# Performance work log

Hardware: AMD Instinct MI355X
Metric: run time of the kernel (lower is better)

Reference implementation:

```python
import jax, jax.numpy as jnp
import numpy as np

BS, Q, S1, S2 = 8, 128, 32, 64
H_DIM, NH = 768, 12
DH = H_DIM // NH


def _linear_params(k, scale=0.02):
    kw, _ = jax.random.split(k)
    w = jax.random.normal(kw, (H_DIM, H_DIM), jnp.float32) * scale
    b = jnp.zeros((H_DIM,), jnp.float32)
    return w, b


def setup_inputs() -> dict:
    root = jax.random.key(0)
    ks = jax.random.split(root, 12)
    wq_w, wq_b = _linear_params(ks[0])
    wk_w, wk_b = _linear_params(ks[1])
    wv_w, wv_b = _linear_params(ks[2])
    sq_w, sq_b = _linear_params(ks[3])
    sk_w, sk_b = _linear_params(ks[4])
    sv_w, sv_b = _linear_params(ks[5])
    return {
        "q_in": jax.random.normal(ks[6], (BS, Q, H_DIM), jnp.float32),
        "k_in": jax.random.normal(ks[7], (BS, S1, S2, H_DIM), jnp.float32),
        "v_in": jax.random.normal(ks[8], (BS, S1, S2, H_DIM), jnp.float32),
        "kvec": jax.random.normal(ks[9], (BS, S1, H_DIM), jnp.float32),
        "word_mask": jnp.ones((BS, S1, S2), jnp.int32),
        "sentence_mask": jnp.ones((BS * Q, S1), jnp.int32),
        "wq_w": wq_w, "wq_b": wq_b, "wk_w": wk_w, "wk_b": wk_b,
        "wv_w": wv_w, "wv_b": wv_b, "sq_w": sq_w, "sq_b": sq_b,
        "sk_w": sk_w, "sk_b": sk_b, "sv_w": sv_w, "sv_b": sv_b,
    }


def reference(q_in, k_in, v_in, kvec, word_mask, sentence_mask,
              wq_w, wq_b, wk_w, wk_b, wv_w, wv_b,
              sq_w, sq_b, sk_w, sk_b, sv_w, sv_b):
    bs, q_len = q_in.shape[0], q_in.shape[1]
    s1, s2 = k_in.shape[1], k_in.shape[2]
    scale = 1.0 / jnp.sqrt(jnp.float32(DH))

    # additive masks, as in the torch module
    wm = (1.0 - word_mask.astype(jnp.float32)) * -10000.0      # [bs, s1, s2]
    sm = (1.0 - sentence_mask.astype(jnp.float32)) * -10000.0  # [bs*Q, s1]

    # ---- word-level attention ----
    q = (q_in @ wq_w + wq_b).reshape(bs, q_len, NH, DH)
    k = (k_in @ wk_w + wk_b).reshape(bs, s1, s2, NH, DH)
    v = (v_in @ wv_w + wv_b).reshape(bs, s1, s2, NH, DH)
    # scores over tokens within each sentence: [bs, s1, H, Q, s2]
    scores1 = jnp.einsum('bqhd,bsthd->bshqt', q, k) * scale
    probs1 = jax.nn.softmax(scores1 + wm[:, :, None, None, :], axis=-1)
    # word_hidden: [bs, Q, s1, h]
    wh = jnp.einsum('bshqt,bsthd->bqshd', probs1, v).reshape(bs, q_len, s1, H_DIM)

    # ---- sentence-level attention ----
    sq = (q_in @ sq_w + sq_b).reshape(bs, q_len, NH, DH)
    sk = (kvec @ sk_w + sk_b).reshape(bs, s1, NH, DH)   # shared across queries
    sv = (wh @ sv_w + sv_b).reshape(bs, q_len, s1, NH, DH)
    scores2 = jnp.einsum('bqhd,bshd->bqhs', sq, sk) * scale  # [bs, Q, H, s1]
    scores2 = scores2 + sm.reshape(bs, q_len, s1)[:, :, None, :]
    probs2 = jax.nn.softmax(scores2, axis=-1)
    out = jnp.einsum('bqhs,bqshd->bqhd', probs2, sv).reshape(bs * q_len, H_DIM)
    return out
```

## Files before the change

### kernel.cpp

```cpp
#include <hip/hip_runtime.h>
#include <hip/hip_bf16.h>


typedef __attribute__((ext_vector_type(8))) short short8;
typedef __attribute__((ext_vector_type(4))) short short4v;
typedef __attribute__((ext_vector_type(4))) float f32x4;

__device__ __forceinline__ short f2bf(float f) {
  __hip_bfloat16 b = __float2bfloat16(f);
  return __builtin_bit_cast(short, b);
}
__device__ __forceinline__ float bf2f(short s) {
  __hip_bfloat16 b = __builtin_bit_cast(__hip_bfloat16, s);
  return __bfloat162float(b);
}

#define MFMA16(a, b, c) __builtin_amdgcn_mfma_f32_16x16x32_bf16((a), (b), (c), 0, 0, 0)

__device__ __forceinline__ void async_load16(const void* g, void* l) {
  auto l3 = (__attribute__((address_space(3))) void*)(uintptr_t)(
      reinterpret_cast<uintptr_t>(l));
  auto g1 = (const __attribute__((address_space(1))) void*)g;
  __builtin_amdgcn_global_load_lds(g1, l3, 16, 0, 0);
}

#define KBAR()                                      \
  do {                                              \
    asm volatile("" ::: "memory");                  \
    __builtin_amdgcn_s_barrier();                   \
    asm volatile("" ::: "memory");                  \
  } while (0)
#define VMW(N) asm volatile("s_waitcnt vmcnt(" #N ")" ::: "memory")

__global__ __launch_bounds__(256)
void prep(const float* __restrict__ w0, const float* __restrict__ w1,
          const float* __restrict__ w2, const float* __restrict__ w3,
          const float* __restrict__ w4, const float* __restrict__ w5,
          short* __restrict__ WT,
          const float* __restrict__ q_in, const float* __restrict__ k_in,
          const float* __restrict__ v_in, const float* __restrict__ kvec,
          short* __restrict__ qbf, short* __restrict__ kbf,
          short* __restrict__ vbf, short* __restrict__ kvb) {
  const int id = blockIdx.x;
  const int tid = threadIdx.x;
  if (id < 3456) {
    __shared__ float tile[32][33];
    const int zz = id / 576, r = id % 576;
    const float* W = (zz == 0) ? w0 : (zz == 1) ? w1 : (zz == 2) ? w2
                   : (zz == 3) ? w3 : (zz == 4) ? w4 : w5;
    short* WTo = WT + (size_t)zz * 768 * 768;
    const int bx = (r % 24) * 32, by = (r / 24) * 32;
    const int tx = tid & 31, ty = tid >> 5;
    #pragma unroll
    for (int i = 0; i < 32; i += 8)
      tile[ty + i][tx] = W[(size_t)(by + ty + i) * 768 + bx + tx];
    __syncthreads();
    #pragma unroll
    for (int i = 0; i < 32; i += 8)
      WTo[(size_t)(bx + ty + i) * 768 + by + tx] = f2bf(tile[tx][ty + i]);
    return;
  }
  const int i = (id - 3456) * 256 + tid;
  const float* src;
  short* dst;
  int idx;
  if (i < 98304)        { src = q_in; dst = qbf; idx = i; }
  else if (i < 1671168) { src = k_in; dst = kbf; idx = i - 98304; }
  else if (i < 3244032) { src = v_in; dst = vbf; idx = i - 1671168; }
  else                  { src = kvec; dst = kvb; idx = i - 3244032; }
  const float4* s = (const float4*)src + (size_t)idx * 2;
  const float4 a = s[0], b = s[1];
  __align__(16) short tmp[8] = {f2bf(a.x), f2bf(a.y), f2bf(a.z), f2bf(a.w),
                                f2bf(b.x), f2bf(b.y), f2bf(b.z), f2bf(b.w)};
  *((short8*)dst + idx) = *(short8*)tmp;
}

__global__ __launch_bounds__(512, 2)
void gemm_proj(const short* __restrict__ kbf, const short* __restrict__ vbf,
               const short* __restrict__ qbf, const short* __restrict__ kvb,
               const short* __restrict__ WT6,
               const float* __restrict__ wk_b, const float* __restrict__ wv_b,
               const float* __restrict__ wq_b, const float* __restrict__ sq_b,
               const float* __restrict__ sk_b,
               short* __restrict__ kp, short* __restrict__ vT,
               short* __restrict__ qp, float* __restrict__ sqp,
               float* __restrict__ skp) {
  const int K = 768, WELEM = 768 * 768;
  extern __shared__ __align__(16) char smem_c[];
  short* smem = (short*)smem_c;
  const int tid = threadIdx.x;
  const int w = tid >> 6, lane = tid & 63, quad = lane >> 4, l16 = lane & 15;
  const f32x4 zero4 = {0.f, 0.f, 0.f, 0.f};

  if (blockIdx.z < 2) {
    short* LA = smem;
    short* LB = smem + 2 * 256 * 64;
    const int z = blockIdx.z;
    const short* Ag = z ? vbf : kbf;
    const short* Bg = z ? (WT6 + 3 * WELEM) : (WT6 + 2 * WELEM);
    const float* bias = z ? wv_b : wk_b;
    const int m0 = blockIdx.x * 256, n0 = blockIdx.y * 256;
    const int wr = w >> 2, wc = w & 3;

    const int srow = lane >> 3;
    const int schk = (lane & 7) ^ srow;
    const short* ag0 = Ag + (size_t)(m0 + w * 8 + srow) * K + schk * 8;
    const short* bg0 = Bg + (size_t)(n0 + w * 8 + srow) * K + schk * 8;
    short* la0 = LA + (w * 8) * 64;
    short* lb0 = LB + (w * 8) * 64;
    const int fsw = l16 & 7;

    f32x4 acc[8][4];
    #pragma unroll
    for (int i = 0; i < 8; i++)
      #pragma unroll
      for (int j = 0; j < 4; j++) acc[i][j] = zero4;

    auto STG1 = [&](int op, int h, int kt) {
      if (kt >= 12) kt -= 2;
      const int buf = kt & 1;
      const short* g = (op ? bg0 : ag0) + (size_t)h * 128 * K + (size_t)kt * 64;
      short* lb = (op ? lb0 : la0) + buf * 16384 + h * (128 * 64);
      async_load16(g, lb);
      async_load16(g + (size_t)64 * K, lb + 64 * 64);
    };

    short8 af[4][2];
    short8 bfr[2][2][2];

#define LDA_(BUF, IH)                                                        \
  _Pragma("unroll") for (int i = 0; i < 4; i++)                              \
    _Pragma("unroll") for (int kb = 0; kb < 2; kb++)                         \
      af[i][kb] = *(const short8*)&LA[(BUF)*16384 +                          \
          (wr * 128 + (IH)*64 + i * 16 + l16) * 64 +                         \
          (((kb * 4 + quad) ^ fsw) * 8)];
#define LDB_(BUF, JH)                                                        \
  _Pragma("unroll") for (int j = 0; j < 2; j++)                              \
    _Pragma("unroll") for (int kb = 0; kb < 2; kb++)                         \
      bfr[JH][j][kb] = *(const short8*)&LB[(BUF)*16384 +                     \
          (wc * 64 + (JH)*32 + j * 16 + l16) * 64 +                          \
          (((kb * 4 + quad) ^ fsw) * 8)];
#define MM_(IH, JH)                                                          \
  __builtin_amdgcn_s_setprio(1);                                             \
  _Pragma("unroll") for (int i = 0; i < 4; i++)                              \
    _Pragma("unroll") for (int j = 0; j < 2; j++) {                          \
      acc[(IH)*4 + i][(JH)*2 + j] =                                          \
          MFMA16(af[i][0], bfr[JH][j][0], acc[(IH)*4 + i][(JH)*2 + j]);      \
      acc[(IH)*4 + i][(JH)*2 + j] =                                          \
          MFMA16(af[i][1], bfr[JH][j][1], acc[(IH)*4 + i][(JH)*2 + j]);      \
    }                                                                        \
  __builtin_amdgcn_s_setprio(0);

    STG1(0, 0, 0); STG1(0, 1, 0); STG1(1, 0, 0); STG1(1, 1, 0);
    STG1(1, 0, 1); STG1(1, 1, 1);
    VMW(4);
    KBAR();

    #pragma unroll 1
    for (int it = 0; it < 6; ++it) {
      const int o = 2 * it + 1, e2 = 2 * it + 2, o2 = 2 * it + 3;
      LDA_(0, 0); LDB_(0, 0); STG1(0, 0, o); KBAR(); MM_(0, 0); KBAR();
      LDB_(0, 1); STG1(0, 1, o); KBAR(); MM_(0, 1); KBAR();
      LDA_(0, 1); STG1(1, 0, e2); KBAR(); MM_(1, 1); KBAR();
      STG1(1, 1, e2); KBAR(); MM_(1, 0); VMW(4); KBAR();
      LDA_(1, 0); LDB_(1, 0); STG1(0, 0, e2); KBAR(); MM_(0, 0); KBAR();
      LDB_(1, 1); STG1(0, 1, e2); KBAR(); MM_(0, 1); KBAR();
      LDA_(1, 1); STG1(1, 0, o2); KBAR(); MM_(1, 1); KBAR();
      STG1(1, 1, o2); KBAR(); MM_(1, 0); VMW(4); KBAR();
    }
#undef LDA_
#undef LDB_
#undef MM_
    VMW(0);

    if (z == 0) {
      #pragma unroll
      for (int I = 0; I < 8; I++)
        #pragma unroll
        for (int J = 0; J < 4; J++) {
          const int col = n0 + wc * 64 + J * 16 + l16;
          const float bv = bias[col];
          #pragma unroll
          for (int r = 0; r < 4; r++) {
            const int g = m0 + wr * 128 + I * 16 + quad * 4 + r;
            kp[(size_t)g * 768 + col] = f2bf(acc[I][J][r] + bv);
          }
        }
    } else {
      const int hh = (n0 >> 6) + wc;
      #pragma unroll
      for (int I = 0; I < 8; I++) {
        const int bs_ = (m0 >> 6) + wr * 2 + (I >> 2);
        const int t0 = (I & 3) * 16 + quad * 4;
        #pragma unroll
        for (int J = 0; J < 4; J++) {
          const int dd = J * 16 + l16;
          const float bv = bias[hh * 64 + dd];
          __align__(8) short tmp[4];
          #pragma unroll
          for (int r = 0; r < 4; r++) tmp[r] = f2bf(acc[I][J][r] + bv);
          *(short4v*)&vT[(((size_t)bs_ * 12 + hh) * 64 + dd) * 64 + t0] =
              *(short4v*)tmp;
        }
      }
    }
    return;
  }

  {
    const int id = blockIdx.x + 64 * blockIdx.y;
    if (id >= 108) return;
    short* As = smem;
    short* Bs = smem + 128 * 32;
    const int qmode = (id < 96);
    const int r = qmode ? id : (id - 96);
    const int bx = qmode ? (r % 8) : (r % 2);
    const int by = qmode ? (r / 8) : (r / 2);
    const short* A = qmode ? qbf : kvb;
    const short* WT = qmode ? (WT6 + 0 * WELEM) : (WT6 + 4 * WELEM);

    const int wm = (w >> 1) * 64, wn = (w & 1) * 64;
    const int m0 = bx * 128, n0 = by * 128;
    const int grow = w * 32 + (lane >> 2);
    const int kc = (lane & 3) * 8;
    const short* ag = A + (size_t)(m0 + grow) * K + kc;
    const short* bg = WT + (size_t)(n0 + grow) * K + kc;
    short* al = &As[(w * 32) * 32];
    short* bl = &Bs[(w * 32) * 32];

    f32x4 acc[4][4];
    #pragma unroll
    for (int i = 0; i < 4; i++)
      #pragma unroll
      for (int j = 0; j < 4; j++) acc[i][j] = zero4;

    for (int k0 = 0; k0 < K; k0 += 32) {
      __syncthreads();
      if (tid < 256) {
        async_load16(ag, al);
        async_load16(ag + (size_t)16 * K, al + 16 * 32);
        async_load16(bg, bl);
        async_load16(bg + (size_t)16 * K, bl + 16 * 32);
      }
      ag += 32;
      bg += 32;
      __syncthreads();
      if (tid < 256) {
        short8 af[4], bf[4];
        #pragma unroll
        for (int i = 0; i < 4; i++)
          af[i] = *(short8*)&As[(wm + i * 16 + l16) * 32 + quad * 8];
        #pragma unroll
        for (int j = 0; j < 4; j++)
          bf[j] = *(short8*)&Bs[(wn + j * 16 + l16) * 32 + quad * 8];
        #pragma unroll
        for (int i = 0; i < 4; i++)
          #pragma unroll
          for (int j = 0; j < 4; j++)
            acc[i][j] = MFMA16(af[i], bf[j], acc[i][j]);
      }
    }
    if (tid >= 256) return;

    #pragma unroll
    for (int i = 0; i < 4; i++) {
      #pragma unroll
      for (int j = 0; j < 4; j++) {
        const int col = n0 + wn + j * 16 + l16;
        const float bv = qmode ? ((col < 768) ? wq_b[col] : sq_b[col - 768])
                               : sk_b[col];
        #pragma unroll
        for (int r4 = 0; r4 < 4; r4++) {
          const int g = m0 + wm + i * 16 + quad * 4 + r4;
          const float v = acc[i][j][r4] + bv;
          if (qmode) {
            if (col < 768) qp[(size_t)g * 768 + col] = f2bf(v * 0.125f);
            else sqp[(size_t)g * 768 + (col - 768)] = v;
          } else {
            skp[(size_t)g * 768 + col] = v;
          }
        }
      }
    }
  }
}

__global__ __launch_bounds__(256)
void wattn_sp(const short* __restrict__ q_proj, const short* __restrict__ k_proj,
              const short* __restrict__ vT, const int* __restrict__ word_mask,
              const float* __restrict__ sq, const float* __restrict__ sk,
              const int* __restrict__ sent_mask, short* __restrict__ wh,
              float* __restrict__ probs2) {
  __shared__ __align__(16) short KVs[128 * 72];
  __shared__ __align__(16) short Ps[128 * 72];
  const int bid = blockIdx.x;
  const int tid = threadIdx.x;

  if (bid >= 3072) {
    float* sc = (float*)KVs;
    const int bq = bid - 3072;
    const int b = bq >> 7, q = bq & 127;
    for (int p = tid; p < 384; p += 256) {
      const int hh = p >> 5, ss = p & 31;
      const float4* a = (const float4*)(sq + ((size_t)(b * 128 + q)) * 768 + hh * 64);
      const float4* c = (const float4*)(sk + ((size_t)(b * 32 + ss)) * 768 + hh * 64);
      float d = 0.f;
      #pragma unroll
      for (int i = 0; i < 16; i++) {
        const float4 av = a[i], cv = c[i];
        d += av.x * cv.x + av.y * cv.y + av.z * cv.z + av.w * cv.w;
      }
      d = d * 0.125f + (1.0f - (float)sent_mask[bq * 32 + ss]) * -10000.0f;
      sc[hh * 33 + ss] = d;
    }
    __syncthreads();
    if (tid < 12) {
      float mx = -3.0e38f;
      for (int ss = 0; ss < 32; ss++) mx = fmaxf(mx, sc[tid * 33 + ss]);
      float sum = 0.f;
      for (int ss = 0; ss < 32; ss++) {
        const float e = __expf(sc[tid * 33 + ss] - mx);
        sc[tid * 33 + ss] = e;
        sum += e;
      }
      const float inv = 1.0f / sum;
      for (int ss = 0; ss < 32; ss++) sc[tid * 33 + ss] *= inv;
    }
    __syncthreads();
    for (int p = tid; p < 384; p += 256) {
      const int hh = p >> 5, ss = p & 31;
      probs2[((size_t)bq * 12 + hh) * 32 + ss] = sc[hh * 33 + ss];
    }
    return;
  }

  short* Ks = KVs;
  short* Vs = KVs + 64 * 72;
  short* Os = KVs;
  const int h = bid % 12, s = (bid / 12) % 32, b = bid / (12 * 32);
  const int w = tid >> 6, lane = tid & 63, quad = lane >> 4, l16 = lane & 15;
  const f32x4 zero4 = {0.f, 0.f, 0.f, 0.f};

  {
    const int t2 = tid & 127;
    const int row8 = t2 >> 3;
    const int c8 = (t2 & 7) * 8;
    if (tid < 128) {
      const short* src = k_proj + ((size_t)((b * 32 + s) * 64)) * 768 + h * 64 + c8;
      #pragma unroll
      for (int i = 0; i < 4; i++) {
        const int r = row8 + i * 16;
        *(short8*)&Ks[r * 72 + c8] = *(const short8*)(src + (size_t)r * 768);
      }
    } else {
      const short* src = vT + ((size_t)((b * 32 + s) * 12 + h)) * 4096 + c8;
      #pragma unroll
      for (int i = 0; i < 4; i++) {
        const int r = row8 + i * 16;
        *(short8*)&Vs[r * 72 + c8] = *(const short8*)(src + (size_t)r * 64);
      }
    }
  }
  __syncthreads();

  f32x4 sac[2][4];
  #pragma unroll
  for (int i = 0; i < 2; i++)
    #pragma unroll
    for (int j = 0; j < 4; j++) sac[i][j] = zero4;
  {
    short8 aq[2][2], bk[4][2];
    #pragma unroll
    for (int i = 0; i < 2; i++)
      #pragma unroll
      for (int kb = 0; kb < 2; kb++)
        aq[i][kb] = *(const short8*)(q_proj +
            ((size_t)(b * 128 + w * 32 + i * 16 + l16)) * 768 + h * 64 + kb * 32 + quad * 8);
    #pragma unroll
    for (int j = 0; j < 4; j++)
      #pragma unroll
      for (int kb = 0; kb < 2; kb++)
        bk[j][kb] = *(short8*)&Ks[(j * 16 + l16) * 72 + kb * 32 + quad * 8];
    #pragma unroll
    for (int i = 0; i < 2; i++)
      #pragma unroll
      for (int j = 0; j < 4; j++) {
        sac[i][j] = MFMA16(aq[i][0], bk[j][0], sac[i][j]);
        sac[i][j] = MFMA16(aq[i][1], bk[j][1], sac[i][j]);
      }
  }

  {
    float wmv[4];
    const int* wmp = word_mask + (b * 32 + s) * 64;
    #pragma unroll
    for (int j = 0; j < 4; j++)
      wmv[j] = (1.0f - (float)wmp[j * 16 + l16]) * -10000.0f;
    #pragma unroll
    for (int i = 0; i < 2; i++) {
      #pragma unroll
      for (int r = 0; r < 4; r++) {
        float vv[4];
        float sum = 0.f;
        #pragma unroll
        for (int j = 0; j < 4; j++) {
          vv[j] = __expf(sac[i][j][r] + wmv[j]);
          sum += vv[j];
        }
        sum += __shfl_xor(sum, 1);
        sum += __shfl_xor(sum, 2);
        sum += __shfl_xor(sum, 4);
        sum += __shfl_xor(sum, 8);
        const float inv = 1.0f / sum;
        const int row = w * 32 + i * 16 + quad * 4 + r;
        #pragma unroll
        for (int j = 0; j < 4; j++)
          Ps[row * 72 + j * 16 + l16] = f2bf(vv[j] * inv);
      }
    }
  }
  __syncthreads();

  f32x4 oac[2][4];
  #pragma unroll
  for (int i = 0; i < 2; i++)
    #pragma unroll
    for (int j = 0; j < 4; j++) oac[i][j] = zero4;
  {
    short8 ap[2][2], bv[4][2];
    #pragma unroll
    for (int i = 0; i < 2; i++)
      #pragma unroll
      for (int kb = 0; kb < 2; kb++)
        ap[i][kb] = *(short8*)&Ps[(w * 32 + i * 16 + l16) * 72 + kb * 32 + quad * 8];
    #pragma unroll
    for (int j = 0; j < 4; j++)
      #pragma unroll
      for (int kb = 0; kb < 2; kb++)
        bv[j][kb] = *(short8*)&Vs[(j * 16 + l16) * 72 + kb * 32 + quad * 8];
    #pragma unroll
    for (int i = 0; i < 2; i++)
      #pragma unroll
      for (int j = 0; j < 4; j++) {
        oac[i][j] = MFMA16(ap[i][0], bv[j][0], oac[i][j]);
        oac[i][j] = MFMA16(ap[i][1], bv[j][1], oac[i][j]);
      }
  }
  __syncthreads();
  #pragma unroll
  for (int i = 0; i < 2; i++)
    #pragma unroll
    for (int j = 0; j < 4; j++)
      #pragma unroll
      for (int r = 0; r < 4; r++)
        Os[(w * 32 + i * 16 + quad * 4 + r) * 72 + j * 16 + l16] = f2bf(oac[i][j][r]);
  __syncthreads();

  {
    const int c8 = (tid & 7) * 8;
    #pragma unroll
    for (int i = 0; i < 4; i++) {
      const int row = i * 32 + (tid >> 3);
      short* dst = wh + (((size_t)(b * 128 + row)) * 32 + s) * 768 + h * 64;
      *(short8*)(dst + c8) = *(const short8*)&Os[row * 72 + c8];
    }
  }
}

__global__ __launch_bounds__(256)
void whc_kernel(const short* __restrict__ wh, const float* __restrict__ probs2,
                short* __restrict__ whc) {
  __shared__ __align__(16) short whs[32 * 776];
  __shared__ float p2s[384];
  const int bq = blockIdx.x, tid = threadIdx.x;
  const short8* src = (const short8*)(wh + (size_t)bq * 24576);
  for (int t = tid; t < 3072; t += 256) {
    const int row = t / 96, c8 = (t % 96) * 8;
    *(short8*)&whs[row * 776 + c8] = src[t];
  }
  for (int p = tid; p < 384; p += 256) p2s[p] = probs2[(size_t)bq * 384 + p];
  __syncthreads();

  float acc[3][12];
  #pragma unroll
  for (int kk = 0; kk < 3; kk++)
    #pragma unroll
    for (int h = 0; h < 12; h++) acc[kk][h] = 0.f;

  for (int s = 0; s < 32; s++) {
    float p2r[12];
    #pragma unroll
    for (int h = 0; h < 12; h++) p2r[h] = p2s[h * 32 + s];
    #pragma unroll
    for (int kk = 0; kk < 3; kk++) {
      const float wv = bf2f(whs[s * 776 + kk * 256 + tid]);
      #pragma unroll
      for (int h = 0; h < 12; h++) acc[kk][h] += p2r[h] * wv;
    }
  }
  #pragma unroll
  for (int h = 0; h < 12; h++)
    #pragma unroll
    for (int kk = 0; kk < 3; kk++)
      whc[((size_t)h * 1024 + bq) * 768 + kk * 256 + tid] = f2bf(acc[kk][h]);
}

__global__ __launch_bounds__(256)
void outg(const short* __restrict__ whc, const short* __restrict__ WTsv,
          const float* __restrict__ sv_b, float* __restrict__ out) {
  const int K = 768;
  __shared__ __align__(16) short As[128 * 32];
  __shared__ __align__(16) short Bs[64 * 32];
  const int tid = threadIdx.x;
  const int m0 = blockIdx.x * 128, h = blockIdx.y;
  const int w = tid >> 6, lane = tid & 63, quad = lane >> 4, l16 = lane & 15;
  const int wm = (w >> 1) * 64, wn = (w & 1) * 32;

  const int grow = w * 32 + (lane >> 2);
  const int kc = (lane & 3) * 8;
  const short* ag = whc + ((size_t)h * 1024 + m0 + grow) * K + kc;
  short* al = &As[(w * 32) * 32];
  const int growb = w * 16 + (lane >> 2);
  const short* bg = WTsv + (size_t)(h * 64 + growb) * K + kc;
  short* bl = &Bs[(w * 16) * 32];

  const f32x4 zero4 = {0.f, 0.f, 0.f, 0.f};
  f32x4 acc[4][2];
  #pragma unroll
  for (int i = 0; i < 4; i++)
    #pragma unroll
    for (int j = 0; j < 2; j++) acc[i][j] = zero4;

  for (int k0 = 0; k0 < K; k0 += 32) {
    __syncthreads();
    async_load16(ag, al);
    async_load16(ag + (size_t)16 * K, al + 16 * 32);
    async_load16(bg, bl);
    ag += 32;
    bg += 32;
    __syncthreads();
    short8 af[4], bf[2];
    #pragma unroll
    for (int i = 0; i < 4; i++)
      af[i] = *(short8*)&As[(wm + i * 16 + l16) * 32 + quad * 8];
    #pragma unroll
    for (int j = 0; j < 2; j++)
      bf[j] = *(short8*)&Bs[(wn + j * 16 + l16) * 32 + quad * 8];
    #pragma unroll
    for (int i = 0; i < 4; i++)
      #pragma unroll
      for (int j = 0; j < 2; j++)
        acc[i][j] = MFMA16(af[i], bf[j], acc[i][j]);
  }

  #pragma unroll
  for (int i = 0; i < 4; i++) {
    #pragma unroll
    for (int j = 0; j < 2; j++) {
      const int col = h * 64 + wn + j * 16 + l16;
      const float bv = sv_b[col];
      #pragma unroll
      for (int r = 0; r < 4; r++) {
        const int g = m0 + wm + i * 16 + quad * 4 + r;
        out[(size_t)g * 768 + col] = acc[i][j][r] + bv;
      }
    }
  }
}

extern "C" void kernel_launch(void* const* d_in, const int* in_sizes, int n_in,
                              void* d_out, int out_size, void* d_ws, size_t ws_size,
                              hipStream_t stream) {
  (void)in_sizes; (void)n_in; (void)out_size; (void)ws_size;
  const float* q_in      = (const float*)d_in[0];
  const float* k_in      = (const float*)d_in[1];
  const float* v_in      = (const float*)d_in[2];
  const float* kvec      = (const float*)d_in[3];
  const int*   word_mask = (const int*)d_in[4];
  const int*   sent_mask = (const int*)d_in[5];
  const float* wq_w = (const float*)d_in[6],  *wq_b = (const float*)d_in[7];
  const float* wk_w = (const float*)d_in[8],  *wk_b = (const float*)d_in[9];
  const float* wv_w = (const float*)d_in[10], *wv_b = (const float*)d_in[11];
  const float* sq_w = (const float*)d_in[12], *sq_b = (const float*)d_in[13];
  const float* sk_w = (const float*)d_in[14], *sk_b = (const float*)d_in[15];
  const float* sv_w = (const float*)d_in[16], *sv_b = (const float*)d_in[17];
  float* out = (float*)d_out;

  const int WELEM = 768 * 768;

  static bool s_attr_done = false;
  if (!s_attr_done) {
    (void)hipFuncSetAttribute(reinterpret_cast<const void*>(&gemm_proj),
                              hipFuncAttributeMaxDynamicSharedMemorySize, 131072);
    s_attr_done = true;
  }

  char* ws = (char*)d_ws;
  size_t off = 0;
  auto alloc = [&](size_t bytes) -> void* {
    void* p = ws + off;
    off += (bytes + 255) & ~(size_t)255;
    return p;
  };
  short* WT  = (short*)alloc((size_t)6 * 768 * 768 * 2);
  short* qbf = (short*)alloc((size_t)1024 * 768 * 2);
  short* kbf = (short*)alloc((size_t)16384 * 768 * 2);
  short* vbf = (short*)alloc((size_t)16384 * 768 * 2);
  short* kvb = (short*)alloc((size_t)256 * 768 * 2);
  short* qp  = (short*)alloc((size_t)1024 * 768 * 2);
  short* kp  = (short*)alloc((size_t)16384 * 768 * 2);
  short* vT  = (short*)alloc((size_t)16384 * 768 * 2);
  float* sqp = (float*)alloc((size_t)1024 * 768 * 4);
  float* skp = (float*)alloc((size_t)256 * 768 * 4);
  short* wh  = (short*)alloc((size_t)32768 * 768 * 2);
  float* pr2 = (float*)alloc((size_t)1024 * 12 * 32 * 4);
  short* whc = (short*)alloc((size_t)12 * 1024 * 768 * 2);

  prep<<<dim3(16224), 256, 0, stream>>>(wq_w, sq_w, wk_w, wv_w, sk_w, sv_w, WT,
                                        q_in, k_in, v_in, kvec, qbf, kbf, vbf, kvb);
  gemm_proj<<<dim3(64, 3, 3), 512, 131072, stream>>>(
      kbf, vbf, qbf, kvb, WT, wk_b, wv_b, wq_b, sq_b, sk_b,
      kp, vT, qp, sqp, skp);
  wattn_sp<<<dim3(4096), 256, 0, stream>>>(qp, kp, vT, word_mask, sqp, skp,
                                           sent_mask, wh, pr2);
  whc_kernel<<<dim3(1024), 256, 0, stream>>>(wh, pr2, whc);
  outg<<<dim3(8, 12), 256, 0, stream>>>(whc, WT + 5 * WELEM, sv_b, out);
}
```

Baseline: 312.2 us.

## Parallelize sentence softmax, hoist Q/mask loads, halve outg tile rows

The sentence-level softmax now spreads each head's 32 scores across 16 lanes and reduces with shuffles, replacing the previous 12-thread serial loop. The word-attention blocks issue their Q-fragment and word-mask global loads before the K/V shared-memory staging so those latencies overlap. The final outg GEMM uses 64-row tiles instead of 128, doubling the grid from 96 to 192 blocks so more compute units are busy, at the cost of more repeated reads of B tiles.

```diff
diff --git a/kernel.cpp b/kernel.cpp
--- a/kernel.cpp
+++ b/kernel.cpp
@@ -314,17 +314,19 @@
       sc[hh * 33 + ss] = d;
     }
     __syncthreads();
-    if (tid < 12) {
-      float mx = -3.0e38f;
-      for (int ss = 0; ss < 32; ss++) mx = fmaxf(mx, sc[tid * 33 + ss]);
-      float sum = 0.f;
-      for (int ss = 0; ss < 32; ss++) {
-        const float e = __expf(sc[tid * 33 + ss] - mx);
-        sc[tid * 33 + ss] = e;
-        sum += e;
-      }
+    if (tid < 192) {
+      const int hh = tid >> 4, l = tid & 15;
+      const float v0 = sc[hh * 33 + l], v1 = sc[hh * 33 + 16 + l];
+      float mx = fmaxf(v0, v1);
+      #pragma unroll
+      for (int d = 1; d < 16; d <<= 1) mx = fmaxf(mx, __shfl_xor(mx, d, 16));
+      const float e0 = __expf(v0 - mx), e1 = __expf(v1 - mx);
+      float sum = e0 + e1;
+      #pragma unroll
+      for (int d = 1; d < 16; d <<= 1) sum += __shfl_xor(sum, d, 16);
       const float inv = 1.0f / sum;
-      for (int ss = 0; ss < 32; ss++) sc[tid * 33 + ss] *= inv;
+      sc[hh * 33 + l] = e0 * inv;
+      sc[hh * 33 + 16 + l] = e1 * inv;
     }
     __syncthreads();
     for (int p = tid; p < 384; p += 256) {
@@ -341,6 +343,21 @@
   const int w = tid >> 6, lane = tid & 63, quad = lane >> 4, l16 = lane & 15;
   const f32x4 zero4 = {0.f, 0.f, 0.f, 0.f};
 
+  short8 aq[2][2];
+  float wmv[4];
+  {
+    #pragma unroll
+    for (int i = 0; i < 2; i++)
+      #pragma unroll
+      for (int kb = 0; kb < 2; kb++)
+        aq[i][kb] = *(const short8*)(q_proj +
+            ((size_t)(b * 128 + w * 32 + i * 16 + l16)) * 768 + h * 64 + kb * 32 + quad * 8);
+    const int* wmp = word_mask + (b * 32 + s) * 64;
+    #pragma unroll
+    for (int j = 0; j < 4; j++)
+      wmv[j] = (1.0f - (float)wmp[j * 16 + l16]) * -10000.0f;
+  }
+
   {
     const int t2 = tid & 127;
     const int row8 = t2 >> 3;
@@ -369,13 +386,7 @@
     #pragma unroll
     for (int j = 0; j < 4; j++) sac[i][j] = zero4;
   {
-    short8 aq[2][2], bk[4][2];
-    #pragma unroll
-    for (int i = 0; i < 2; i++)
-      #pragma unroll
-      for (int kb = 0; kb < 2; kb++)
-        aq[i][kb] = *(const short8*)(q_proj +
-            ((size_t)(b * 128 + w * 32 + i * 16 + l16)) * 768 + h * 64 + kb * 32 + quad * 8);
+    short8 bk[4][2];
     #pragma unroll
     for (int j = 0; j < 4; j++)
       #pragma unroll
@@ -391,11 +402,6 @@
   }
 
   {
-    float wmv[4];
-    const int* wmp = word_mask + (b * 32 + s) * 64;
-    #pragma unroll
-    for (int j = 0; j < 4; j++)
-      wmv[j] = (1.0f - (float)wmp[j * 16 + l16]) * -10000.0f;
     #pragma unroll
     for (int i = 0; i < 2; i++) {
       #pragma unroll
@@ -509,60 +515,58 @@
 void outg(const short* __restrict__ whc, const short* __restrict__ WTsv,
           const float* __restrict__ sv_b, float* __restrict__ out) {
   const int K = 768;
-  __shared__ __align__(16) short As[128 * 32];
+  __shared__ __align__(16) short As[64 * 32];
   __shared__ __align__(16) short Bs[64 * 32];
   const int tid = threadIdx.x;
-  const int m0 = blockIdx.x * 128, h = blockIdx.y;
+  const int m0 = blockIdx.x * 64, h = blockIdx.y;
   const int w = tid >> 6, lane = tid & 63, quad = lane >> 4, l16 = lane & 15;
-  const int wm = (w >> 1) * 64, wn = (w & 1) * 32;
-
-  const int grow = w * 32 + (lane >> 2);
+  const int wm = (w >> 1) * 32, wn = (w & 1) * 32;
+
+  const int grow = w * 16 + (lane >> 2);
   const int kc = (lane & 3) * 8;
   const short* ag = whc + ((size_t)h * 1024 + m0 + grow) * K + kc;
-  short* al = &As[(w * 32) * 32];
-  const int growb = w * 16 + (lane >> 2);
-  const short* bg = WTsv + (size_t)(h * 64 + growb) * K + kc;
+  short* al = &As[(w * 16) * 32];
+  const short* bg = WTsv + (size_t)(h * 64 + grow) * K + kc;
   short* bl = &Bs[(w * 16) * 32];
 
   const f32x4 zero4 = {0.f, 0.f, 0.f, 0.f};
-  f32x4 acc[4][2];
+  f32x4 acc[2][2];
   #pragma unroll
-  for (int i = 0; i < 4; i++)
+  for (int i = 0; i < 2; i++)
     #pragma unroll
     for (int j = 0; j < 2; j++) acc[i][j] = zero4;
 
   for (int k0 = 0; k0 < K; k0 += 32) {
     __syncthreads();
     async_load16(ag, al);
-    async_load16(ag + (size_t)16 * K, al + 16 * 32);
     async_load16(bg, bl);
     ag += 32;
     bg += 32;
     __syncthreads();
-    short8 af[4], bf[2];
-    #pragma unroll
-    for (int i = 0; i < 4; i++)
+    short8 af[2], bf[2];
+    #pragma unroll
+    for (int i = 0; i < 2; i++)
       af[i] = *(short8*)&As[(wm + i * 16 + l16) * 32 + quad * 8];
     #pragma unroll
     for (int j = 0; j < 2; j++)
       bf[j] = *(short8*)&Bs[(wn + j * 16 + l16) * 32 + quad * 8];
     #pragma unroll
-    for (int i = 0; i < 4; i++)
+    for (int i = 0; i < 2; i++)
       #pragma unroll
       for (int j = 0; j < 2; j++)
         acc[i][j] = MFMA16(af[i], bf[j], acc[i][j]);
   }
 
   #pragma unroll
-  for (int i = 0; i < 4; i++) {
+  for (int i = 0; i < 2; i++) {
     #pragma unroll
     for (int j = 0; j < 2; j++) {
       const int col = h * 64 + wn + j * 16 + l16;
       const float bv = sv_b[col];
       #pragma unroll
-      for (int r = 0; r < 4; r++) {
+      for (int r = 0; r < 2 * 2; r++) {
         const int g = m0 + wm + i * 16 + quad * 4 + r;
-        out[(size_t)g * 768 + col] = acc[i][j][r] + bv;
+        if (r < 4) out[(size_t)g * 768 + col] = acc[i][j][r] + bv;
       }
     }
   }
@@ -624,5 +628,5 @@
   wattn_sp<<<dim3(4096), 256, 0, stream>>>(qp, kp, vT, word_mask, sqp, skp,
                                            sent_mask, wh, pr2);
   whc_kernel<<<dim3(1024), 256, 0, stream>>>(wh, pr2, whc);
-  outg<<<dim3(8, 12), 256, 0, stream>>>(whc, WT + 5 * WELEM, sv_b, out);
-}
+  outg<<<dim3(16, 12), 256, 0, stream>>>(whc, WT + 5 * WELEM, sv_b, out);
+}
```

New measurement: 303.8 us. -2.7%, faster.
